# Kernel tuning notes

Measured on AMD Instinct MI355X. Metric: run time of the kernel, lower is better.

The kernel has to match this reference:

```python
import jax, jax.numpy as jnp
import numpy as np

B, C, D = 16384, 512, 512
EXT = 2
H = C * EXT
TAU = 1.0          # temperature_train
STEP = 0.05        # langevin_step_size
NOISE = 0.1        # langevin_noise
STEPS = 32         # langevin_steps


def setup_inputs() -> dict:
    key = jax.random.key(0)
    ks = jax.random.split(key, 8)
    s_in = 1.0 / np.sqrt(D)
    s_h = 1.0 / np.sqrt(H)
    return {
        'x': jax.random.normal(ks[0], (B, D), jnp.float32),
        'vanilla_components': jnp.abs(jax.random.normal(ks[1], (C, D), jnp.float32) * 0.1),
        'e_sp': jax.random.normal(ks[2], (C * D,), jnp.float32) * 0.1,
        'W1e': jax.random.normal(ks[3], (D, H), jnp.float32) * s_in,
        'b1e': jnp.zeros((H,), jnp.float32),
        'W2e': jax.random.normal(ks[4], (H, C), jnp.float32) * s_h,
        'b2e': jnp.zeros((C,), jnp.float32),
        'W1r': jax.random.normal(ks[5], (D, H), jnp.float32) * s_in,
        'b1r': jnp.zeros((H,), jnp.float32),
        'W2r': jax.random.normal(ks[6], (H, C), jnp.float32) * s_h,
        'b2r': jnp.zeros((C,), jnp.float32),
    }


def _langevin_gate(e, key):
    """Langevin MCMC on latent u with quadratic energy E(u)=0.5||u||^2 + <e,u>.
    Returns selection probability sigmoid(-u/tau)."""
    def step(u, k):
        grad = u + e  # dE/du
        u = u - STEP * grad + NOISE * jax.random.normal(k, u.shape, u.dtype)
        return u, None
    u, _ = jax.lax.scan(step, jnp.zeros_like(e), jax.random.split(key, STEPS))
    return jax.nn.sigmoid(-u / TAU)


def reference(x, vanilla_components, e_sp, W1e, b1e, W2e, b2e, W1r, b1r, W2r, b2r):
    k1, k2 = jax.random.split(jax.random.key(42))
    # non-negative components
    comps = jnp.abs(vanilla_components)  # [C, D]
    # fixed energy-based sparsity mask over component entries
    p_sp = _langevin_gate(e_sp, k1).reshape(C, D)
    comps = comps * p_sp
    # dynamic per-sample component selection energies via MLP
    h = jax.nn.relu(x @ W1e + b1e)          # [B, H]
    e_dyn = h @ W2e + b2e                   # [B, C]
    gate = _langevin_gate(e_dyn, k2)        # [B, C] soft gates (train mode)
    hr = jax.nn.relu(x @ W1r + b1r)         # [B, H]
    conc = (hr @ W2r + b2r) * gate          # [B, C]
    # aggregate: (concentration * components).sum over components -> [B, D]
    return conc @ comps
```

## Files before the change

kernel.cpp:

```cpp
#include <hip/hip_runtime.h>
#include <hip/hip_bf16.h>
#include <stdint.h>

#define Bn 16384
#define Cn 512
#define Dn 512
#define Hn 1024

#define A32 0.80628851f

typedef __attribute__((ext_vector_type(8))) short bf16x8;
typedef __attribute__((ext_vector_type(4))) float f32x4;
typedef __attribute__((ext_vector_type(2))) float f32x2;

__device__ __forceinline__ ushort f2bf(float f) {
  uint32_t u = __float_as_uint(f);
  return (ushort)((u + 0x7fffu + ((u >> 16) & 1u)) >> 16);
}
__device__ __forceinline__ float b2f(ushort u) {
  return __uint_as_float((uint32_t)u << 16);
}

constexpr uint32_t crotl(uint32_t v, int s) {
  return (v << s) | (v >> (32 - s));
}
struct TFOut { uint32_t w0, w1; };
constexpr TFOut ctf(uint32_t k0, uint32_t k1, uint32_t x0, uint32_t x1) {
  const uint32_t ks[3] = {k0, k1, k0 ^ k1 ^ 0x1BD11BDAu};
  const int rot[8] = {13, 15, 26, 6, 17, 29, 16, 24};
  uint32_t a = x0 + k0, b = x1 + k1;
  for (int g = 0; g < 5; ++g) {
    for (int i = 0; i < 4; ++i) {
      int r = rot[(g & 1) * 4 + i];
      a += b; b = crotl(b, r); b ^= a;
    }
    a += ks[(g + 1) % 3];
    b += ks[(g + 2) % 3] + (uint32_t)(g + 1);
  }
  return {a, b};
}
struct KeySched { uint32_t s[64]; uint32_t d[64]; };
constexpr KeySched make_keys() {
  KeySched K{};
  TFOut k1 = ctf(0u, 42u, 0u, 0u);
  TFOut k2 = ctf(0u, 42u, 0u, 1u);
  for (uint32_t t = 0; t < 32; ++t) {
    TFOut ws = ctf(k1.w0, k1.w1, 0u, t);
    K.s[2 * t] = ws.w0; K.s[2 * t + 1] = ws.w1;
    TFOut wd = ctf(k2.w0, k2.w1, 0u, t);
    K.d[2 * t] = wd.w0; K.d[2 * t + 1] = wd.w1;
  }
  return K;
}
constexpr KeySched KS = make_keys();

__device__ __forceinline__ uint32_t rotl32(uint32_t v, int s) {
  return __builtin_rotateleft32(v, (uint32_t)s);
}
__device__ __forceinline__ uint32_t tf_xor(uint32_t K0, uint32_t K1,
                                           uint32_t KX, uint32_t j) {
  uint32_t a = K0, b = K1 + j;
#define TR(r) { a += b; b = rotl32(b, (r)); b ^= a; }
  TR(13) TR(15) TR(26) TR(6)   a += K1; b += KX + 1u;
  TR(17) TR(29) TR(16) TR(24)  a += KX; b += K0 + 2u;
  TR(13) TR(15) TR(26) TR(6)   a += K0; b += K1 + 3u;
  TR(17) TR(29) TR(16) TR(24)  a += K1; b += KX + 4u;
  TR(13) TR(15) TR(26) TR(6)   a += KX; b += K0 + 5u;
#undef TR
  return a ^ b;
}

__device__ __forceinline__ float bits_to_normal(uint32_t bits) {
  float f = __uint_as_float((bits >> 9) | 0x3f800000u) - 1.0f;
  float x = f * 2.0f - 0x1.fffffep-1f;
  float w = -__logf(1.0f - x * x);
  float p;
  if (w < 5.0f) {
    w -= 2.5f;
    p =            2.81022636e-08f;
    p = fmaf(p, w, 3.43273939e-07f);
    p = fmaf(p, w, -3.5233877e-06f);
    p = fmaf(p, w, -4.39150654e-06f);
    p = fmaf(p, w, 0.00021858087f);
    p = fmaf(p, w, -0.00125372503f);
    p = fmaf(p, w, -0.00417768164f);
    p = fmaf(p, w, 0.246640727f);
    p = fmaf(p, w, 1.50140941f);
  } else {
    w = sqrtf(w) - 3.0f;
    p =            -0.000200214257f;
    p = fmaf(p, w, 0.000100950558f);
    p = fmaf(p, w, 0.00134934322f);
    p = fmaf(p, w, -0.00367342844f);
    p = fmaf(p, w, 0.00573950773f);
    p = fmaf(p, w, -0.0076224613f);
    p = fmaf(p, w, 0.00943887047f);
    p = fmaf(p, w, 1.00167406f);
    p = fmaf(p, w, 2.83297682f);
  }
  return 0x1.6a09e6p+0f * (p * x);
}

__global__ __launch_bounds__(256) void k_smask(
    const float* __restrict__ vc, const float* __restrict__ e_sp,
    ushort* __restrict__ compsT) {
  uint32_t jj = blockIdx.x * 256 + threadIdx.x;
  uint32_t c = jj & (Cn - 1), d = jj >> 9;
  uint32_t ridx = c * Dn + d;
  float e = e_sp[ridx];
  float u = 0.0f;
#pragma unroll
  for (int t = 0; t < 32; ++t) {
    const uint32_t K0 = KS.s[2 * t], K1 = KS.s[2 * t + 1];
    uint32_t s = tf_xor(K0, K1, K0 ^ K1 ^ 0x1BD11BDAu, ridx);
    float n = bits_to_normal(s);
    u = (u - 0.05f * (u + e)) + 0.1f * n;
  }
  float gt = 1.0f / (1.0f + __expf(u));
  compsT[jj] = f2bf(fabsf(vc[ridx]) * gt);
}

__device__ __forceinline__ void zdyn_block(ushort* __restrict__ Z, uint32_t rb) {
  const uint32_t j = rb * 256u + threadIdx.x;
  float z = 0.0f;
#pragma unroll
  for (int t = 0; t < 32; t += 2) {
    const uint32_t Ka0 = KS.d[2 * t],     Ka1 = KS.d[2 * t + 1];
    const uint32_t Kb0 = KS.d[2 * t + 2], Kb1 = KS.d[2 * t + 3];
    uint32_t s0 = tf_xor(Ka0, Ka1, Ka0 ^ Ka1 ^ 0x1BD11BDAu, j);
    uint32_t s1 = tf_xor(Kb0, Kb1, Kb0 ^ Kb1 ^ 0x1BD11BDAu, j);
    float f0 = __uint_as_float((s0 >> 9) | 0x3f800000u) - 1.0f;
    float f1 = __uint_as_float((s1 >> 9) | 0x3f800000u) - 1.0f;
    float x0 = f0 * 2.0f - 0x1.fffffep-1f;
    float x1 = f1 * 2.0f - 0x1.fffffep-1f;
    float w0 = fminf(-__logf(fmaf(-x0, x0, 1.0f)), 5.0f) - 2.5f;
    float w1 = fminf(-__logf(fmaf(-x1, x1, 1.0f)), 5.0f) - 2.5f;
    f32x2 X = {x0, x1}, W = {w0, w1};
    f32x2 P = {2.81022636e-08f, 2.81022636e-08f};
    P = __builtin_elementwise_fma(P, W, (f32x2){3.43273939e-07f, 3.43273939e-07f});
    P = __builtin_elementwise_fma(P, W, (f32x2){-3.5233877e-06f, -3.5233877e-06f});
    P = __builtin_elementwise_fma(P, W, (f32x2){-4.39150654e-06f, -4.39150654e-06f});
    P = __builtin_elementwise_fma(P, W, (f32x2){0.00021858087f, 0.00021858087f});
    P = __builtin_elementwise_fma(P, W, (f32x2){-0.00125372503f, -0.00125372503f});
    P = __builtin_elementwise_fma(P, W, (f32x2){-0.00417768164f, -0.00417768164f});
    P = __builtin_elementwise_fma(P, W, (f32x2){0.246640727f, 0.246640727f});
    P = __builtin_elementwise_fma(P, W, (f32x2){1.50140941f, 1.50140941f});
    f32x2 Q = (P * X) * (f32x2){0.14142135f, 0.14142135f};
    z = fmaf(0.95f, z, Q.x);
    z = fmaf(0.95f, z, Q.y);
  }
  Z[j] = f2bf(z);
}

__device__ __forceinline__ void gemm_tile_bf(
    const ushort* __restrict__ A, const ushort* __restrict__ WT,
    const float* __restrict__ bias, ushort* __restrict__ Out, int g,
    ushort As[128][40], ushort Bs[128][40]) {
  const int n0 = (g & 7) * 128, m0 = (g >> 3) * 128;
  const int t = threadIdx.x;
  const int srow = t >> 1, skb = (t & 1) << 4;
  const ushort* Ap = A  + (size_t)(m0 + srow) * Dn + skb;
  const ushort* Bp = WT + (size_t)(n0 + srow) * Dn + skb;
  const int wave = t >> 6, lane = t & 63;
  const int wm = (wave >> 1) << 6, wn = (wave & 1) << 6;
  const int quad = lane >> 4, l15 = lane & 15;

  f32x4 acc[4][4] = {};
  for (int k0 = 0; k0 < Dn; k0 += 32) {
    uint4 a0 = *(const uint4*)(Ap + k0);
    uint4 a1 = *(const uint4*)(Ap + k0 + 8);
    uint4 b0 = *(const uint4*)(Bp + k0);
    uint4 b1 = *(const uint4*)(Bp + k0 + 8);
    *(uint4*)&As[srow][skb] = a0; *(uint4*)&As[srow][skb + 8] = a1;
    *(uint4*)&Bs[srow][skb] = b0; *(uint4*)&Bs[srow][skb + 8] = b1;
    __syncthreads();
    bf16x8 af[4], bfr[4];
#pragma unroll
    for (int i = 0; i < 4; ++i) {
      af[i] = *(const bf16x8*)&As[wm + i * 16 + l15][quad * 8];
      bfr[i] = *(const bf16x8*)&Bs[wn + i * 16 + l15][quad * 8];
    }
#pragma unroll
    for (int i = 0; i < 4; ++i)
#pragma unroll
      for (int j = 0; j < 4; ++j)
        acc[i][j] = __builtin_amdgcn_mfma_f32_16x16x32_bf16(af[i], bfr[j],
                                                            acc[i][j], 0, 0, 0);
    __syncthreads();
  }
#pragma unroll
  for (int i = 0; i < 4; ++i)
#pragma unroll
    for (int j = 0; j < 4; ++j) {
      const int col = n0 + wn + j * 16 + l15;
      const float bv = bias[col];
#pragma unroll
      for (int r = 0; r < 4; ++r) {
        const int row = m0 + wm + i * 16 + quad * 4 + r;
        Out[(size_t)row * Hn + col] = f2bf(fmaxf(acc[i][j][r] + bv, 0.0f));
      }
    }
}

__global__ __launch_bounds__(256) void k_mega2(
    const ushort* __restrict__ x_bf,
    const ushort* __restrict__ W1eT, const float* __restrict__ b1e,
    ushort* __restrict__ h,
    const ushort* __restrict__ W1rT, const float* __restrict__ b1r,
    ushort* __restrict__ hr,
    ushort* __restrict__ Zdyn) {
  __shared__ ushort As[128][40];
  __shared__ ushort Bs[128][40];
  const uint32_t bx = blockIdx.x;
  const uint32_t group = bx / 34u, pos = bx % 34u;
  if (pos == 0u)
    gemm_tile_bf(x_bf, W1eT, b1e, h, (int)group, As, Bs);
  else if (pos == 1u)
    gemm_tile_bf(x_bf, W1rT, b1r, hr, (int)group, As, Bs);
  else
    zdyn_block(Zdyn, group * 32u + (pos - 2u));
}

__global__ __launch_bounds__(256) void k_cvt_x(const float* __restrict__ in,
                                               ushort* __restrict__ out) {
  int i = (blockIdx.x * 256 + threadIdx.x) * 4;
  float4 v = *(const float4*)(in + i);
  *(ushort4*)(out + i) = make_ushort4(f2bf(v.x), f2bf(v.y), f2bf(v.z), f2bf(v.w));
}

__global__ __launch_bounds__(256) void k_transpose_cvt(
    const float* __restrict__ in, ushort* __restrict__ out, int NO, int KO) {
  int o = blockIdx.x * 256 + threadIdx.x;
  int n = o / KO, k = o % KO;
  out[o] = f2bf(in[(size_t)k * NO + n]);
}

__global__ __launch_bounds__(256) void k_dgemm(
    const ushort* __restrict__ h, const ushort* __restrict__ W2eT,
    const float* __restrict__ b2e,
    const ushort* __restrict__ hr, const ushort* __restrict__ W2rT,
    const float* __restrict__ b2r,
    ushort* __restrict__ Zconc) {
  __shared__ ushort As[128][40];
  __shared__ ushort Bs[128][40];
  const int t = threadIdx.x;
  const int m0 = blockIdx.y * 128, n0 = blockIdx.x * 128;
  const int srow = t >> 1, skb = (t & 1) << 4;
  const int wave = t >> 6, lane = t & 63;
  const int wm = (wave >> 1) << 6, wn = (wave & 1) << 6;
  const int quad = lane >> 4, l15 = lane & 15;

  const ushort* Ap = h    + (size_t)(m0 + srow) * Hn + skb;
  const ushort* Bp = W2eT + (size_t)(n0 + srow) * Hn + skb;
  f32x4 acc[4][4] = {};
  for (int k0 = 0; k0 < Hn; k0 += 32) {
    uint4 a0 = *(const uint4*)(Ap + k0);
    uint4 a1 = *(const uint4*)(Ap + k0 + 8);
    uint4 b0 = *(const uint4*)(Bp + k0);
    uint4 b1 = *(const uint4*)(Bp + k0 + 8);
    *(uint4*)&As[srow][skb] = a0; *(uint4*)&As[srow][skb + 8] = a1;
    *(uint4*)&Bs[srow][skb] = b0; *(uint4*)&Bs[srow][skb + 8] = b1;
    __syncthreads();
    bf16x8 af[4], bfr[4];
#pragma unroll
    for (int i = 0; i < 4; ++i) {
      af[i] = *(const bf16x8*)&As[wm + i * 16 + l15][quad * 8];
      bfr[i] = *(const bf16x8*)&Bs[wn + i * 16 + l15][quad * 8];
    }
#pragma unroll
    for (int i = 0; i < 4; ++i)
#pragma unroll
      for (int j = 0; j < 4; ++j)
        acc[i][j] = __builtin_amdgcn_mfma_f32_16x16x32_bf16(af[i], bfr[j],
                                                            acc[i][j], 0, 0, 0);
    __syncthreads();
  }
  float g[4][4][4];
#pragma unroll
  for (int i = 0; i < 4; ++i)
#pragma unroll
    for (int j = 0; j < 4; ++j) {
      const int col = n0 + wn + j * 16 + l15;
      const float bv = b2e[col];
#pragma unroll
      for (int r = 0; r < 4; ++r) {
        const int row = m0 + wm + i * 16 + quad * 4 + r;
        float e = acc[i][j][r] + bv;
        float z = b2f(Zconc[(size_t)row * Cn + col]);
        g[i][j][r] = 1.0f / (1.0f + __expf(z - A32 * e));
        acc[i][j][r] = 0.0f;
      }
    }
  Ap = hr   + (size_t)(m0 + srow) * Hn + skb;
  Bp = W2rT + (size_t)(n0 + srow) * Hn + skb;
  for (int k0 = 0; k0 < Hn; k0 += 32) {
    uint4 a0 = *(const uint4*)(Ap + k0);
    uint4 a1 = *(const uint4*)(Ap + k0 + 8);
    uint4 b0 = *(const uint4*)(Bp + k0);
    uint4 b1 = *(const uint4*)(Bp + k0 + 8);
    __syncthreads();
    *(uint4*)&As[srow][skb] = a0; *(uint4*)&As[srow][skb + 8] = a1;
    *(uint4*)&Bs[srow][skb] = b0; *(uint4*)&Bs[srow][skb + 8] = b1;
    __syncthreads();
    bf16x8 af[4], bfr[4];
#pragma unroll
    for (int i = 0; i < 4; ++i) {
      af[i] = *(const bf16x8*)&As[wm + i * 16 + l15][quad * 8];
      bfr[i] = *(const bf16x8*)&Bs[wn + i * 16 + l15][quad * 8];
    }
#pragma unroll
    for (int i = 0; i < 4; ++i)
#pragma unroll
      for (int j = 0; j < 4; ++j)
        acc[i][j] = __builtin_amdgcn_mfma_f32_16x16x32_bf16(af[i], bfr[j],
                                                            acc[i][j], 0, 0, 0);
  }
#pragma unroll
  for (int i = 0; i < 4; ++i)
#pragma unroll
    for (int j = 0; j < 4; ++j) {
      const int col = n0 + wn + j * 16 + l15;
      const float bv = b2r[col];
#pragma unroll
      for (int r = 0; r < 4; ++r) {
        const int row = m0 + wm + i * 16 + quad * 4 + r;
        Zconc[(size_t)row * Cn + col] = f2bf((acc[i][j][r] + bv) * g[i][j][r]);
      }
    }
}

__global__ __launch_bounds__(256) void k_gemm_out(
    const ushort* __restrict__ A, const ushort* __restrict__ WT,
    float* __restrict__ Out) {
  __shared__ ushort As[128][40];
  __shared__ ushort Bs[128][40];
  const int t = threadIdx.x;
  const int m0 = blockIdx.y * 128, n0 = blockIdx.x * 128;
  const int srow = t >> 1, skb = (t & 1) << 4;
  const ushort* Ap = A  + (size_t)(m0 + srow) * Cn + skb;
  const ushort* Bp = WT + (size_t)(n0 + srow) * Cn + skb;
  const int wave = t >> 6, lane = t & 63;
  const int wm = (wave >> 1) << 6, wn = (wave & 1) << 6;
  const int quad = lane >> 4, l15 = lane & 15;

  f32x4 acc[4][4] = {};
  for (int k0 = 0; k0 < Cn; k0 += 32) {
    uint4 a0 = *(const uint4*)(Ap + k0);
    uint4 a1 = *(const uint4*)(Ap + k0 + 8);
    uint4 b0 = *(const uint4*)(Bp + k0);
    uint4 b1 = *(const uint4*)(Bp + k0 + 8);
    *(uint4*)&As[srow][skb] = a0; *(uint4*)&As[srow][skb + 8] = a1;
    *(uint4*)&Bs[srow][skb] = b0; *(uint4*)&Bs[srow][skb + 8] = b1;
    __syncthreads();
    bf16x8 af[4], bfr[4];
#pragma unroll
    for (int i = 0; i < 4; ++i) {
      af[i] = *(const bf16x8*)&As[wm + i * 16 + l15][quad * 8];
      bfr[i] = *(const bf16x8*)&Bs[wn + i * 16 + l15][quad * 8];
    }
#pragma unroll
    for (int i = 0; i < 4; ++i)
#pragma unroll
      for (int j = 0; j < 4; ++j)
        acc[i][j] = __builtin_amdgcn_mfma_f32_16x16x32_bf16(af[i], bfr[j],
                                                            acc[i][j], 0, 0, 0);
    __syncthreads();
  }
#pragma unroll
  for (int i = 0; i < 4; ++i)
#pragma unroll
    for (int j = 0; j < 4; ++j) {
      const int col = n0 + wn + j * 16 + l15;
#pragma unroll
      for (int r = 0; r < 4; ++r) {
        const int row = m0 + wm + i * 16 + quad * 4 + r;
        Out[(size_t)row * Dn + col] = acc[i][j][r];
      }
    }
}

extern "C" void kernel_launch(void* const* d_in, const int* in_sizes, int n_in,
                              void* d_out, int out_size, void* d_ws, size_t ws_size,
                              hipStream_t stream) {
  const float* x    = (const float*)d_in[0];
  const float* vc   = (const float*)d_in[1];
  const float* e_sp = (const float*)d_in[2];
  const float* W1e  = (const float*)d_in[3];
  const float* b1e  = (const float*)d_in[4];
  const float* W2e  = (const float*)d_in[5];
  const float* b2e  = (const float*)d_in[6];
  const float* W1r  = (const float*)d_in[7];
  const float* b1r  = (const float*)d_in[8];
  const float* W2r  = (const float*)d_in[9];
  const float* b2r  = (const float*)d_in[10];
  float* out = (float*)d_out;

  char* ws = (char*)d_ws;
  ushort* W1eT   = (ushort*)(ws + (1u << 12));
  ushort* W2eT   = (ushort*)(ws + (1u << 12) + (1u << 20));
  ushort* W1rT   = (ushort*)(ws + (1u << 12) + (2u << 20));
  ushort* W2rT   = (ushort*)(ws + (1u << 12) + (3u << 20));
  ushort* compsT = (ushort*)(ws + (1u << 12) + (4u << 20));
  ushort* Zdyn   = (ushort*)(ws + (8u << 20));
  ushort* h_bf   = (ushort*)(ws + (24u << 20));
  ushort* hr_bf  = (ushort*)(ws + (56u << 20));
  ushort* x_bf   = (ushort*)d_out;

  k_cvt_x<<<(Bn * Dn / 4) / 256, 256, 0, stream>>>(x, x_bf);
  k_transpose_cvt<<<(Dn * Hn) / 256, 256, 0, stream>>>(W1e, W1eT, Hn, Dn);
  k_transpose_cvt<<<(Hn * Cn) / 256, 256, 0, stream>>>(W2e, W2eT, Cn, Hn);
  k_transpose_cvt<<<(Dn * Hn) / 256, 256, 0, stream>>>(W1r, W1rT, Hn, Dn);
  k_transpose_cvt<<<(Hn * Cn) / 256, 256, 0, stream>>>(W2r, W2rT, Cn, Hn);
  k_smask<<<(Cn * Dn) / 256, 256, 0, stream>>>(vc, e_sp, compsT);
  k_mega2<<<34816, 256, 0, stream>>>(x_bf, W1eT, b1e, h_bf, W1rT, b1r, hr_bf,
                                     Zdyn);
  k_dgemm<<<dim3(Cn / 128, Bn / 128), 256, 0, stream>>>(
      h_bf, W2eT, b2e, hr_bf, W2rT, b2r, Zdyn);
  k_gemm_out<<<dim3(Dn / 128, Bn / 128), 256, 0, stream>>>(Zdyn, compsT, out);
}
```

Baseline: 878.8 us.

## Merge prep kernels, tile weight transposes, split Langevin noise out of GEMM mega-kernel

The six small prep launches (x conversion, four weight transposes, sparsity mask) become one k_prep kernel. The transposes now go through a 32x33 shared-memory tile so reads and writes are coalesced. The Langevin noise accumulation is taken out of the mixed GEMM/noise mega-kernel and runs as its own k_z kernel, where each thread handles two elements with an interleaved inline Threefry to raise ILP. The first-layer GEMMs get a dedicated launch. This cuts launch overhead and uncoalesced transpose traffic, but the noise work no longer overlaps with the GEMM tiles inside one kernel.

```diff
diff --git a/kernel.cpp b/kernel.cpp
--- a/kernel.cpp
+++ b/kernel.cpp
@@ -101,34 +101,29 @@
   return 0x1.6a09e6p+0f * (p * x);
 }
 
-__global__ __launch_bounds__(256) void k_smask(
-    const float* __restrict__ vc, const float* __restrict__ e_sp,
-    ushort* __restrict__ compsT) {
-  uint32_t jj = blockIdx.x * 256 + threadIdx.x;
-  uint32_t c = jj & (Cn - 1), d = jj >> 9;
-  uint32_t ridx = c * Dn + d;
-  float e = e_sp[ridx];
-  float u = 0.0f;
+__global__ __launch_bounds__(256) void k_z(ushort* __restrict__ Z) {
+  const uint32_t j0 = (blockIdx.x * 256u + threadIdx.x) * 2u;
+  const uint32_t j1 = j0 + 1u;
+  float z0 = 0.0f, z1 = 0.0f;
 #pragma unroll
   for (int t = 0; t < 32; ++t) {
-    const uint32_t K0 = KS.s[2 * t], K1 = KS.s[2 * t + 1];
-    uint32_t s = tf_xor(K0, K1, K0 ^ K1 ^ 0x1BD11BDAu, ridx);
-    float n = bits_to_normal(s);
-    u = (u - 0.05f * (u + e)) + 0.1f * n;
-  }
-  float gt = 1.0f / (1.0f + __expf(u));
-  compsT[jj] = f2bf(fabsf(vc[ridx]) * gt);
-}
-
-__device__ __forceinline__ void zdyn_block(ushort* __restrict__ Z, uint32_t rb) {
-  const uint32_t j = rb * 256u + threadIdx.x;
-  float z = 0.0f;
-#pragma unroll
-  for (int t = 0; t < 32; t += 2) {
-    const uint32_t Ka0 = KS.d[2 * t],     Ka1 = KS.d[2 * t + 1];
-    const uint32_t Kb0 = KS.d[2 * t + 2], Kb1 = KS.d[2 * t + 3];
-    uint32_t s0 = tf_xor(Ka0, Ka1, Ka0 ^ Ka1 ^ 0x1BD11BDAu, j);
-    uint32_t s1 = tf_xor(Kb0, Kb1, Kb0 ^ Kb1 ^ 0x1BD11BDAu, j);
+    const uint32_t K0 = KS.d[2 * t], K1 = KS.d[2 * t + 1];
+    const uint32_t KX = K0 ^ K1 ^ 0x1BD11BDAu;
+    uint32_t a0 = K0, b0 = K1 + j0;
+    uint32_t a1 = K0, b1 = K1 + j1;
+#define R2(r)                                                  \
+    a0 += b0; a1 += b1;                                        \
+    b0 = rotl32(b0, (r)); b1 = rotl32(b1, (r));                \
+    b0 ^= a0; b1 ^= a1;
+#define I2(p, q) a0 += (p); a1 += (p); b0 += (q); b1 += (q);
+    R2(13) R2(15) R2(26) R2(6)  I2(K1, KX + 1u)
+    R2(17) R2(29) R2(16) R2(24) I2(KX, K0 + 2u)
+    R2(13) R2(15) R2(26) R2(6)  I2(K0, K1 + 3u)
+    R2(17) R2(29) R2(16) R2(24) I2(K1, KX + 4u)
+    R2(13) R2(15) R2(26) R2(6)  I2(KX, K0 + 5u)
+#undef R2
+#undef I2
+    uint32_t s0 = a0 ^ b0, s1 = a1 ^ b1;
     float f0 = __uint_as_float((s0 >> 9) | 0x3f800000u) - 1.0f;
     float f1 = __uint_as_float((s1 >> 9) | 0x3f800000u) - 1.0f;
     float x0 = f0 * 2.0f - 0x1.fffffep-1f;
@@ -146,10 +141,73 @@
     P = __builtin_elementwise_fma(P, W, (f32x2){0.246640727f, 0.246640727f});
     P = __builtin_elementwise_fma(P, W, (f32x2){1.50140941f, 1.50140941f});
     f32x2 Q = (P * X) * (f32x2){0.14142135f, 0.14142135f};
-    z = fmaf(0.95f, z, Q.x);
-    z = fmaf(0.95f, z, Q.y);
-  }
-  Z[j] = f2bf(z);
+    z0 = fmaf(0.95f, z0, Q.x);
+    z1 = fmaf(0.95f, z1, Q.y);
+  }
+  *(ushort2*)(Z + j0) = make_ushort2(f2bf(z0), f2bf(z1));
+}
+
+__device__ __forceinline__ void transpose_tile(
+    const float* __restrict__ in, ushort* __restrict__ out,
+    int N, int K, int tIdx, float T[32][33]) {
+  const int ntn = N / 32;
+  const int tk = tIdx / ntn, tn = tIdx % ntn;
+  const int tx = threadIdx.x & 31, ty = threadIdx.x >> 5;
+  const int k0 = tk * 32, n0 = tn * 32;
+#pragma unroll
+  for (int r = 0; r < 32; r += 8)
+    T[ty + r][tx] = in[(size_t)(k0 + ty + r) * N + n0 + tx];
+  __syncthreads();
+#pragma unroll
+  for (int r = 0; r < 32; r += 8)
+    out[(size_t)(n0 + ty + r) * K + k0 + tx] = f2bf(T[tx][ty + r]);
+}
+
+__device__ __forceinline__ void smask_block(
+    const float* __restrict__ vc, const float* __restrict__ e_sp,
+    ushort* __restrict__ compsT, int g) {
+  uint32_t jj = (uint32_t)g * 256 + threadIdx.x;
+  uint32_t c = jj & (Cn - 1), d = jj >> 9;
+  uint32_t ridx = c * Dn + d;
+  float e = e_sp[ridx];
+  float u = 0.0f;
+#pragma unroll
+  for (int t = 0; t < 32; ++t) {
+    const uint32_t K0 = KS.s[2 * t], K1 = KS.s[2 * t + 1];
+    uint32_t s = tf_xor(K0, K1, K0 ^ K1 ^ 0x1BD11BDAu, ridx);
+    float n = bits_to_normal(s);
+    u = (u - 0.05f * (u + e)) + 0.1f * n;
+  }
+  float gt = 1.0f / (1.0f + __expf(u));
+  compsT[jj] = f2bf(fabsf(vc[ridx]) * gt);
+}
+
+__global__ __launch_bounds__(256) void k_prep(
+    const float* __restrict__ x, ushort* __restrict__ x_bf,
+    const float* __restrict__ W1e, ushort* __restrict__ W1eT,
+    const float* __restrict__ W2e, ushort* __restrict__ W2eT,
+    const float* __restrict__ W1r, ushort* __restrict__ W1rT,
+    const float* __restrict__ W2r, ushort* __restrict__ W2rT,
+    const float* __restrict__ vc, const float* __restrict__ e_sp,
+    ushort* __restrict__ compsT) {
+  __shared__ float T[32][33];
+  const int pos = blockIdx.x;
+  if (pos < 8192) {
+    int i = (pos * 256 + threadIdx.x) * 4;
+    float4 v = *(const float4*)(x + i);
+    *(ushort4*)(x_bf + i) =
+        make_ushort4(f2bf(v.x), f2bf(v.y), f2bf(v.z), f2bf(v.w));
+  } else if (pos < 8704) {
+    transpose_tile(W1e, W1eT, Hn, Dn, pos - 8192, T);
+  } else if (pos < 9216) {
+    transpose_tile(W2e, W2eT, Cn, Hn, pos - 8704, T);
+  } else if (pos < 9728) {
+    transpose_tile(W1r, W1rT, Hn, Dn, pos - 9216, T);
+  } else if (pos < 10240) {
+    transpose_tile(W2r, W2rT, Cn, Hn, pos - 9728, T);
+  } else {
+    smask_block(vc, e_sp, compsT, pos - 10240);
+  }
 }
 
 __device__ __forceinline__ void gemm_tile_bf(
@@ -202,37 +260,20 @@
     }
 }
 
-__global__ __launch_bounds__(256) void k_mega2(
+__global__ __launch_bounds__(256) void k_g13(
     const ushort* __restrict__ x_bf,
     const ushort* __restrict__ W1eT, const float* __restrict__ b1e,
     ushort* __restrict__ h,
     const ushort* __restrict__ W1rT, const float* __restrict__ b1r,
-    ushort* __restrict__ hr,
-    ushort* __restrict__ Zdyn) {
+    ushort* __restrict__ hr) {
   __shared__ ushort As[128][40];
   __shared__ ushort Bs[128][40];
-  const uint32_t bx = blockIdx.x;
-  const uint32_t group = bx / 34u, pos = bx % 34u;
-  if (pos == 0u)
-    gemm_tile_bf(x_bf, W1eT, b1e, h, (int)group, As, Bs);
-  else if (pos == 1u)
-    gemm_tile_bf(x_bf, W1rT, b1r, hr, (int)group, As, Bs);
+  const int pos = blockIdx.x;
+  const int g = pos >> 1;
+  if (pos & 1)
+    gemm_tile_bf(x_bf, W1rT, b1r, hr, g, As, Bs);
   else
-    zdyn_block(Zdyn, group * 32u + (pos - 2u));
-}
-
-__global__ __launch_bounds__(256) void k_cvt_x(const float* __restrict__ in,
-                                               ushort* __restrict__ out) {
-  int i = (blockIdx.x * 256 + threadIdx.x) * 4;
-  float4 v = *(const float4*)(in + i);
-  *(ushort4*)(out + i) = make_ushort4(f2bf(v.x), f2bf(v.y), f2bf(v.z), f2bf(v.w));
-}
-
-__global__ __launch_bounds__(256) void k_transpose_cvt(
-    const float* __restrict__ in, ushort* __restrict__ out, int NO, int KO) {
-  int o = blockIdx.x * 256 + threadIdx.x;
-  int n = o / KO, k = o % KO;
-  out[o] = f2bf(in[(size_t)k * NO + n]);
+    gemm_tile_bf(x_bf, W1eT, b1e, h, g, As, Bs);
 }
 
 __global__ __launch_bounds__(256) void k_dgemm(
@@ -406,14 +447,10 @@
   ushort* hr_bf  = (ushort*)(ws + (56u << 20));
   ushort* x_bf   = (ushort*)d_out;
 
-  k_cvt_x<<<(Bn * Dn / 4) / 256, 256, 0, stream>>>(x, x_bf);
-  k_transpose_cvt<<<(Dn * Hn) / 256, 256, 0, stream>>>(W1e, W1eT, Hn, Dn);
-  k_transpose_cvt<<<(Hn * Cn) / 256, 256, 0, stream>>>(W2e, W2eT, Cn, Hn);
-  k_transpose_cvt<<<(Dn * Hn) / 256, 256, 0, stream>>>(W1r, W1rT, Hn, Dn);
-  k_transpose_cvt<<<(Hn * Cn) / 256, 256, 0, stream>>>(W2r, W2rT, Cn, Hn);
-  k_smask<<<(Cn * Dn) / 256, 256, 0, stream>>>(vc, e_sp, compsT);
-  k_mega2<<<34816, 256, 0, stream>>>(x_bf, W1eT, b1e, h_bf, W1rT, b1r, hr_bf,
-                                     Zdyn);
+  k_prep<<<11264, 256, 0, stream>>>(x, x_bf, W1e, W1eT, W2e, W2eT,
+                                    W1r, W1rT, W2r, W2rT, vc, e_sp, compsT);
+  k_z<<<16384, 256, 0, stream>>>(Zdyn);
+  k_g13<<<2048, 256, 0, stream>>>(x_bf, W1eT, b1e, h_bf, W1rT, b1r, hr_bf);
   k_dgemm<<<dim3(Cn / 128, Bn / 128), 256, 0, stream>>>(
       h_bf, W2eT, b2e, hr_bf, W2rT, b2r, Zdyn);
   k_gemm_out<<<dim3(Dn / 128, Bn / 128), 256, 0, stream>>>(Zdyn, compsT, out);
```

Result: faster. 835.1 us (-5.0%).
